# Performance work log

Measured on AMD Instinct MI355X. Metric: run time of the kernel, lower is better.

Reference implementation:

```python
import jax, jax.numpy as jnp
import numpy as np

W = 2  # config.spatial_width in NeuTraj


def _offsets():
    d = np.arange(-W, W + 1)
    dx, dy = np.meshgrid(d, d, indexing='ij')
    return jnp.asarray(np.stack([dx.ravel(), dy.ravel()], axis=1))  # [(2W+1)^2, 2]


def setup_inputs() -> dict:
    key = jax.random.key(0)
    ks = jax.random.split(key, 10)
    B, H, F = 8192, 128, 128
    G = 1100
    N = G + 3 * W  # 1106
    stdv = 1.0 / np.sqrt(H)
    u = lambda k, s: jax.random.uniform(k, s, jnp.float32, -stdv, stdv)
    return {
        'input_feat': jax.random.normal(ks[0], (B, F), jnp.float32),
        'hx': jax.random.normal(ks[1], (B, H), jnp.float32),
        'grid_idx': jax.random.randint(ks[2], (B, 2), 0, G),
        'memory': jax.random.normal(ks[3], (N, N, H), jnp.float32) * 0.1,
        'w_ih': u(ks[4], (4 * H, F)),
        'w_hh': u(ks[5], (4 * H, H)),
        'b_ih': u(ks[6], (4 * H,)),
        'b_hh': u(ks[7], (4 * H,)),
        'w_out': u(ks[8], (H, 2 * H)),  # Attention.linear_out
        'b_out': u(ks[9], (H,)),
    }


def reference(input_feat, hx, grid_idx, memory, w_ih, w_hh, b_ih, b_hh, w_out, b_out):
    g = grid_idx + W  # shift by spatial_width, as in the torch code
    # GRU-style gate GEMMs (4 gates: reset, update, new, spatial)
    gi = input_feat @ w_ih.T + b_ih
    gh = hx @ w_hh.T + b_hh
    i_r, i_i, i_n, i_s = jnp.split(gi, 4, axis=1)
    h_r, h_i, h_n, h_s = jnp.split(gh, 4, axis=1)
    resetgate = jax.nn.sigmoid(i_r + h_r)
    updategate = jax.nn.sigmoid(i_i + h_i)
    spatialgate = jax.nn.sigmoid(i_s + h_s)
    newgate = jnp.tanh(i_n + resetgate * h_n)

    # cy_hh = newgate.data  -> detached attention query
    q = jax.lax.stop_gradient(newgate)

    # gather (2W+1)^2 = 25 neighboring grid cells per sample: cs [B, 25, H]
    nb = g[:, None, :] + _offsets()[None]  # [B, 25, 2]
    cs = memory[nb[..., 0], nb[..., 1]]

    # Luong attention: scores -> softmax -> mix -> concat -> linear -> tanh
    scores = jnp.einsum('bh,blh->bl', q, cs)
    attn = jax.nn.softmax(scores, axis=1)
    mix = jnp.einsum('bl,blh->bh', attn, cs)
    combined = jnp.concatenate([mix, q], axis=1)  # [B, 2H]
    atten_cs = jnp.tanh(combined @ w_out.T + b_out)

    curr_state = newgate + spatialgate * atten_cs
    hyy = curr_state + updategate * (hx - curr_state)

    # incell scatter write-back (all .data in torch -> stop_gradient)
    sg = jax.lax.stop_gradient(spatialgate)
    cd = jax.lax.stop_gradient(hyy)
    gx, gy = g[:, 0], g[:, 1]
    updates = sg * memory[gx, gy] + (1.0 - sg) * cd
    new_memory = memory.at[gx, gy].set(jax.lax.stop_gradient(updates))
    return hyy, new_memory
```

## Files before the change

kernel.cpp:

```cpp
#include <hip/hip_runtime.h>
#include <hip/hip_bf16.h>

typedef float f32x4 __attribute__((ext_vector_type(4)));

#define B_  8192
#define H_  128
#define NW  1106
#define NC  640
#define KK  256

static const size_t N4TOT = (size_t)NW * NW * H_ / 4;

#define SL_A 2000000UL
#define SL_B 6000000UL
#define SL_C 5000000UL
#define SL_D 2000000UL

#define PREP_CB  512
#define PREP_CPB 768
#define GEMM_CPB 1024
#define ATTN_CPB 4096
#define FIN_BLKS 2048

__device__ __forceinline__ float sigmf(float x) { return 1.0f / (1.0f + expf(-x)); }

__device__ __forceinline__ void copy_span(const f32x4* __restrict__ src,
                                          f32x4* __restrict__ dst,
                                          size_t lo, size_t hi,
                                          size_t ctid, size_t cthreads) {
    for (size_t i = lo + ctid; i < hi; i += cthreads) {
        f32x4 v = __builtin_nontemporal_load(src + i);
        __builtin_nontemporal_store(v, dst + i);
    }
}

__global__ __launch_bounds__(256) void prep_kernel(
    const float* __restrict__ xf, const float* __restrict__ hx,
    const float* __restrict__ w_ih, const float* __restrict__ w_hh,
    float* __restrict__ Z, float* __restrict__ Wbig, int* __restrict__ winner,
    const f32x4* __restrict__ src, f32x4* __restrict__ dst, size_t lo, size_t hi) {
    int bid = blockIdx.x, tid = threadIdx.x;
    if (bid >= PREP_CB) {
        size_t ctid = (size_t)(bid - PREP_CB) * 256 + tid;
        copy_span(src, dst, lo, hi, ctid, (size_t)(gridDim.x - PREP_CB) * 256);
        return;
    }
    size_t stride = (size_t)PREP_CB * 256;
    size_t id0 = (size_t)bid * 256 + tid;
    for (size_t i = id0; i < (size_t)B_ * 256; i += stride) {
        size_t b = i >> 8; int c = (int)(i & 255);
        Z[i] = (c < 128) ? xf[b * 128 + c] : hx[b * 128 + (c - 128)];
    }
    for (size_t i = id0; i < (size_t)NC * 256; i += stride) {
        int j = (int)(i >> 8); int k = (int)(i & 255);
        float v;
        if (j < 256) {
            v = (k < 128) ? w_ih[j * 128 + k] : w_hh[j * 128 + (k - 128)];
        } else if (j < 384) {
            int r = 384 + (j - 256);
            v = (k < 128) ? w_ih[r * 128 + k] : w_hh[r * 128 + (k - 128)];
        } else if (j < 512) {
            int r = 256 + (j - 384);
            v = (k < 128) ? w_ih[r * 128 + k] : 0.0f;
        } else {
            int r = 256 + (j - 512);
            v = (k < 128) ? 0.0f : w_hh[r * 128 + (k - 128)];
        }
        Wbig[i] = v;
    }
    for (size_t i = id0; i < (size_t)NW * NW; i += stride) winner[i] = -1;
}

__global__ __launch_bounds__(256) void gemm_abt(
    const float* __restrict__ A, const float* __restrict__ Bw,
    float* __restrict__ Cc, int ldc, int nx, int nxny,
    const int* __restrict__ gidx, int* __restrict__ winner,
    const f32x4* __restrict__ src, f32x4* __restrict__ dst, size_t lo, size_t hi) {
    __shared__ float As[64][36];
    __shared__ float Ws[32][132];
    int bid = blockIdx.x, tid = threadIdx.x;
    if (bid >= nxny) {
        int rel = bid - nxny;
        if (gidx != nullptr && rel < 32) {
            int b = rel * 256 + tid;
            int gx = gidx[2 * b] + 2, gy = gidx[2 * b + 1] + 2;
            atomicMax(&winner[gx * NW + gy], b);
        }
        size_t ctid = (size_t)rel * 256 + tid;
        copy_span(src, dst, lo, hi, ctid, (size_t)(gridDim.x - nxny) * 256);
        return;
    }
    int bx = bid % nx, by = bid / nx;
    int tn = tid & 15, tm = tid >> 4;
    size_t m0 = (size_t)bx * 64;
    int n0 = by * 128;
    float acc[4][8];
#pragma unroll
    for (int i = 0; i < 4; ++i)
#pragma unroll
        for (int j = 0; j < 8; ++j) acc[i][j] = 0.0f;

    for (int k0 = 0; k0 < KK; k0 += 32) {
        __syncthreads();
#pragma unroll
        for (int p = 0; p < 2; ++p) {
            int f = tid + 256 * p; int r = f >> 3, cq = f & 7;
            float4 v = *(const float4*)(A + (m0 + r) * KK + (k0 + 4 * cq));
            *(float4*)(&As[r][4 * cq]) = v;
        }
#pragma unroll
        for (int p = 0; p < 4; ++p) {
            int f = tid + 256 * p; int c = f >> 3, cq = f & 7;
            float4 v = *(const float4*)(Bw + (size_t)(n0 + c) * KK + (k0 + 4 * cq));
            Ws[4 * cq + 0][c] = v.x; Ws[4 * cq + 1][c] = v.y;
            Ws[4 * cq + 2][c] = v.z; Ws[4 * cq + 3][c] = v.w;
        }
        __syncthreads();
#pragma unroll
        for (int kk = 0; kk < 32; ++kk) {
            float4 w0 = *(const float4*)(&Ws[kk][4 * tn]);
            float4 w1 = *(const float4*)(&Ws[kk][64 + 4 * tn]);
#pragma unroll
            for (int i = 0; i < 4; ++i) {
                float a = As[4 * tm + i][kk];
                acc[i][0] += a * w0.x; acc[i][1] += a * w0.y;
                acc[i][2] += a * w0.z; acc[i][3] += a * w0.w;
                acc[i][4] += a * w1.x; acc[i][5] += a * w1.y;
                acc[i][6] += a * w1.z; acc[i][7] += a * w1.w;
            }
        }
    }
#pragma unroll
    for (int i = 0; i < 4; ++i) {
        size_t row = m0 + 4 * tm + i;
        float4 v0 = make_float4(acc[i][0], acc[i][1], acc[i][2], acc[i][3]);
        float4 v1 = make_float4(acc[i][4], acc[i][5], acc[i][6], acc[i][7]);
        *(float4*)(Cc + row * ldc + n0 + 4 * tn) = v0;
        *(float4*)(Cc + row * ldc + n0 + 64 + 4 * tn) = v1;
    }
}

__global__ __launch_bounds__(64) void attn_kernel(
    const float* __restrict__ C, const float* __restrict__ memory,
    const int* __restrict__ gidx, const float* __restrict__ b_ih,
    const float* __restrict__ b_hh, float* __restrict__ mixq,
    float* __restrict__ ug, float* __restrict__ sg,
    const f32x4* __restrict__ src, f32x4* __restrict__ dst, size_t lo, size_t hi) {
    int bid = blockIdx.x;
    int t = threadIdx.x;
    if (bid >= B_) {
        size_t ctid = (size_t)(bid - B_) * 64 + t;
        copy_span(src, dst, lo, hi, ctid, (size_t)(gridDim.x - B_) * 64);
        return;
    }
    int b = bid;
    int t1 = t + 64;
    const float* Crow = C + (size_t)b * NC;
    float r0 = sigmf(Crow[t]        + b_ih[t]        + b_hh[t]);
    float r1 = sigmf(Crow[t1]       + b_ih[t1]       + b_hh[t1]);
    float u0 = sigmf(Crow[128 + t]  + b_ih[128 + t]  + b_hh[128 + t]);
    float u1 = sigmf(Crow[128 + t1] + b_ih[128 + t1] + b_hh[128 + t1]);
    float s0 = sigmf(Crow[256 + t]  + b_ih[384 + t]  + b_hh[384 + t]);
    float s1 = sigmf(Crow[256 + t1] + b_ih[384 + t1] + b_hh[384 + t1]);
    float n0 = tanhf(Crow[384 + t]  + b_ih[256 + t]  + r0 * (Crow[512 + t]  + b_hh[256 + t]));
    float n1 = tanhf(Crow[384 + t1] + b_ih[256 + t1] + r1 * (Crow[512 + t1] + b_hh[256 + t1]));

    int gx = gidx[2 * b] + 2, gy = gidx[2 * b + 1] + 2;
    const float* base = memory + ((size_t)gx * NW + gy) * H_ + t;
    float cs0[25], cs1[25];
#pragma unroll
    for (int l = 0; l < 25; ++l) {
        int dx = l / 5 - 2, dy = l % 5 - 2;
        const float* row = base + ((long)dx * NW + dy) * H_;
        cs0[l] = row[0];
        cs1[l] = row[64];
    }
    float sc[25];
#pragma unroll
    for (int l = 0; l < 25; ++l) {
        float p = n0 * cs0[l] + n1 * cs1[l];
#pragma unroll
        for (int w = 1; w < 64; w <<= 1) p += __shfl_xor(p, w, 64);
        sc[l] = p;
    }
    float mx = sc[0];
#pragma unroll
    for (int l = 1; l < 25; ++l) mx = fmaxf(mx, sc[l]);
    float den = 0.0f, mix0 = 0.0f, mix1 = 0.0f;
#pragma unroll
    for (int l = 0; l < 25; ++l) {
        float e = expf(sc[l] - mx);
        den += e;
        mix0 += e * cs0[l];
        mix1 += e * cs1[l];
    }
    float inv = 1.0f / den;
    mix0 *= inv; mix1 *= inv;

    float* mq = mixq + (size_t)b * 256;
    mq[t] = mix0; mq[t1] = mix1; mq[128 + t] = n0; mq[128 + t1] = n1;
    ug[(size_t)b * H_ + t] = u0; ug[(size_t)b * H_ + t1] = u1;
    sg[(size_t)b * H_ + t] = s0; sg[(size_t)b * H_ + t1] = s1;
}

__global__ void copy_kernel(const f32x4* __restrict__ src, f32x4* __restrict__ dst, size_t n4) {
    size_t stride = (size_t)gridDim.x * blockDim.x;
    for (size_t i = (size_t)blockIdx.x * blockDim.x + threadIdx.x; i < n4; i += stride) {
        f32x4 v = __builtin_nontemporal_load(src + i);
        __builtin_nontemporal_store(v, dst + i);
    }
}

__global__ __launch_bounds__(256) void final_kernel(
    const float* __restrict__ AC, const float* __restrict__ b_out,
    const float* __restrict__ sg, const float* __restrict__ ug,
    const float* __restrict__ mixq, const float* __restrict__ hx,
    const float* __restrict__ memory, const int* __restrict__ gidx,
    const int* __restrict__ winner, float* __restrict__ hyy,
    float* __restrict__ newmem,
    const f32x4* __restrict__ src, f32x4* __restrict__ dst, size_t lo, size_t hi) {
    size_t gt = (size_t)blockIdx.x * blockDim.x + threadIdx.x;
    size_t nthr = (size_t)gridDim.x * blockDim.x;
    for (size_t i = gt; i < (size_t)B_ * H_; i += nthr) {
        int b = (int)(i >> 7), t = (int)(i & 127);
        float atten = tanhf(AC[i] + b_out[t]);
        float s = sg[i], u = ug[i];
        float q = mixq[(size_t)b * 256 + 128 + t];
        float curr = q + s * atten;
        float hy = curr + u * (hx[i] - curr);
        hyy[i] = hy;
        int gx = gidx[2 * b] + 2, gy = gidx[2 * b + 1] + 2;
        size_t cell = (size_t)gx * NW + gy;
        if (winner[cell] == b) {
            float m = memory[cell * H_ + t];
            newmem[cell * H_ + t] = s * m + (1.0f - s) * hy;
        }
    }
    for (size_t i = lo + gt; i < hi; i += nthr) {
        if (winner[i >> 5] < 0) {
            f32x4 v = __builtin_nontemporal_load(src + i);
            __builtin_nontemporal_store(v, dst + i);
        }
    }
}

extern "C" void kernel_launch(void* const* d_in, const int* in_sizes, int n_in,
                              void* d_out, int out_size, void* d_ws, size_t ws_size,
                              hipStream_t stream) {
    const float* xf     = (const float*)d_in[0];
    const float* hx     = (const float*)d_in[1];
    const int*   gidx   = (const int*)d_in[2];
    const float* memory = (const float*)d_in[3];
    const float* w_ih   = (const float*)d_in[4];
    const float* w_hh   = (const float*)d_in[5];
    const float* b_ih   = (const float*)d_in[6];
    const float* b_hh   = (const float*)d_in[7];
    const float* w_out  = (const float*)d_in[8];
    const float* b_out  = (const float*)d_in[9];

    float* out    = (float*)d_out;
    float* hyy    = out;
    float* newmem = out + (size_t)B_ * H_;
    const f32x4* src4 = (const f32x4*)memory;
    f32x4*       dst4 = (f32x4*)newmem;

    float* wsf    = (float*)d_ws;
    float* mixq   = wsf;
    float* ug     = mixq + (size_t)B_ * 256;
    float* sg     = ug + (size_t)B_ * H_;
    float* AC     = sg + (size_t)B_ * H_;
    int*   winner = (int*)(AC + (size_t)B_ * H_);
    char*  pers_end = (char*)(winner + (size_t)NW * NW);
    size_t pers_bytes = (size_t)(pers_end - (char*)d_ws);

    size_t ZF = (size_t)B_ * 256, CF = (size_t)B_ * NC, WBF = (size_t)NC * 256;
    size_t trans_bytes = (ZF + CF + WBF) * sizeof(float);
    bool distributed = (ws_size >= pers_bytes + trans_bytes);
    float* trans = distributed ? (float*)pers_end : newmem;
    float* Z    = trans;
    float* Cbuf = Z + ZF;
    float* Wbig = Cbuf + CF;

    if (distributed) {
        size_t a1 = SL_A, b1 = a1 + SL_B, c1 = b1 + SL_C, d1 = c1 + SL_D;
        prep_kernel<<<PREP_CB + PREP_CPB, 256, 0, stream>>>(
            xf, hx, w_ih, w_hh, Z, Wbig, winner, src4, dst4, 0, a1);
        gemm_abt<<<640 + GEMM_CPB, 256, 0, stream>>>(
            Z, Wbig, Cbuf, NC, 128, 640, gidx, winner, src4, dst4, a1, b1);
        attn_kernel<<<B_ + ATTN_CPB, 64, 0, stream>>>(
            Cbuf, memory, gidx, b_ih, b_hh, mixq, ug, sg, src4, dst4, b1, c1);
        gemm_abt<<<128 + GEMM_CPB, 256, 0, stream>>>(
            mixq, w_out, AC, H_, 128, 128, nullptr, winner, src4, dst4, c1, d1);
        final_kernel<<<FIN_BLKS, 256, 0, stream>>>(
            AC, b_out, sg, ug, mixq, hx, memory, gidx, winner, hyy, newmem,
            src4, dst4, d1, N4TOT);
    } else {
        prep_kernel<<<PREP_CB, 256, 0, stream>>>(
            xf, hx, w_ih, w_hh, Z, Wbig, winner, src4, dst4, 0, 0);
        gemm_abt<<<640 + 32, 256, 0, stream>>>(
            Z, Wbig, Cbuf, NC, 128, 640, gidx, winner, src4, dst4, 0, 0);
        attn_kernel<<<B_, 64, 0, stream>>>(
            Cbuf, memory, gidx, b_ih, b_hh, mixq, ug, sg, src4, dst4, 0, 0);
        gemm_abt<<<128, 256, 0, stream>>>(
            mixq, w_out, AC, H_, 128, 128, nullptr, winner, src4, dst4, 0, 0);
        copy_kernel<<<2048, 256, 0, stream>>>(src4, dst4, N4TOT);
        final_kernel<<<FIN_BLKS, 256, 0, stream>>>(
            AC, b_out, sg, ug, mixq, hx, memory, gidx, winner, hyy, newmem,
            src4, dst4, 0, 0);
    }
}
```

Baseline: 281.9 us.

## Collapse five-stage pipeline into three kernels with fused GEMM epilogues

After: 333.5 us. 18.3% more time.

```diff
diff --git a/kernel.cpp b/kernel.cpp
--- a/kernel.cpp
+++ b/kernel.cpp
@@ -11,16 +11,13 @@
 
 static const size_t N4TOT = (size_t)NW * NW * H_ / 4;
 
-#define SL_A 2000000UL
-#define SL_B 6000000UL
-#define SL_C 5000000UL
-#define SL_D 2000000UL
-
-#define PREP_CB  512
-#define PREP_CPB 768
-#define GEMM_CPB 1024
-#define ATTN_CPB 4096
-#define FIN_BLKS 2048
+#define SL1 6000000UL
+#define SL2 4000000UL
+
+#define K1_CPB 1024
+#define K2_CB  2048
+#define K2_CPB 1024
+#define K3_CPB 2048
 
 __device__ __forceinline__ float sigmf(float x) { return 1.0f / (1.0f + expf(-x)); }
 
@@ -34,84 +31,57 @@
     }
 }
 
-__global__ __launch_bounds__(256) void prep_kernel(
+__global__ __launch_bounds__(256) void k1_gates(
     const float* __restrict__ xf, const float* __restrict__ hx,
     const float* __restrict__ w_ih, const float* __restrict__ w_hh,
-    float* __restrict__ Z, float* __restrict__ Wbig, int* __restrict__ winner,
-    const f32x4* __restrict__ src, f32x4* __restrict__ dst, size_t lo, size_t hi) {
-    int bid = blockIdx.x, tid = threadIdx.x;
-    if (bid >= PREP_CB) {
-        size_t ctid = (size_t)(bid - PREP_CB) * 256 + tid;
-        copy_span(src, dst, lo, hi, ctid, (size_t)(gridDim.x - PREP_CB) * 256);
-        return;
-    }
-    size_t stride = (size_t)PREP_CB * 256;
-    size_t id0 = (size_t)bid * 256 + tid;
-    for (size_t i = id0; i < (size_t)B_ * 256; i += stride) {
-        size_t b = i >> 8; int c = (int)(i & 255);
-        Z[i] = (c < 128) ? xf[b * 128 + c] : hx[b * 128 + (c - 128)];
-    }
-    for (size_t i = id0; i < (size_t)NC * 256; i += stride) {
-        int j = (int)(i >> 8); int k = (int)(i & 255);
-        float v;
-        if (j < 256) {
-            v = (k < 128) ? w_ih[j * 128 + k] : w_hh[j * 128 + (k - 128)];
-        } else if (j < 384) {
-            int r = 384 + (j - 256);
-            v = (k < 128) ? w_ih[r * 128 + k] : w_hh[r * 128 + (k - 128)];
-        } else if (j < 512) {
-            int r = 256 + (j - 384);
-            v = (k < 128) ? w_ih[r * 128 + k] : 0.0f;
-        } else {
-            int r = 256 + (j - 512);
-            v = (k < 128) ? 0.0f : w_hh[r * 128 + (k - 128)];
-        }
-        Wbig[i] = v;
-    }
-    for (size_t i = id0; i < (size_t)NW * NW; i += stride) winner[i] = -1;
-}
-
-__global__ __launch_bounds__(256) void gemm_abt(
-    const float* __restrict__ A, const float* __restrict__ Bw,
-    float* __restrict__ Cc, int ldc, int nx, int nxny,
-    const int* __restrict__ gidx, int* __restrict__ winner,
+    float* __restrict__ Cbuf, const int* __restrict__ gidx, int* __restrict__ winner,
     const f32x4* __restrict__ src, f32x4* __restrict__ dst, size_t lo, size_t hi) {
     __shared__ float As[64][36];
     __shared__ float Ws[32][132];
     int bid = blockIdx.x, tid = threadIdx.x;
-    if (bid >= nxny) {
-        int rel = bid - nxny;
-        if (gidx != nullptr && rel < 32) {
+    if (bid >= 640) {
+        int rel = bid - 640;
+        if (rel < 32) {
             int b = rel * 256 + tid;
             int gx = gidx[2 * b] + 2, gy = gidx[2 * b + 1] + 2;
             atomicMax(&winner[gx * NW + gy], b);
         }
         size_t ctid = (size_t)rel * 256 + tid;
-        copy_span(src, dst, lo, hi, ctid, (size_t)(gridDim.x - nxny) * 256);
+        copy_span(src, dst, lo, hi, ctid, (size_t)(gridDim.x - 640) * 256);
         return;
     }
-    int bx = bid % nx, by = bid / nx;
+    int bx = bid & 127;
+    int strip = bid >> 7;
+    size_t m0 = (size_t)bx * 64;
+    int n0 = strip * 128;
+    int wbase = (strip == 0) ? 0 : (strip == 1) ? 128 : (strip == 2) ? 384 : 256;
+    int kstart = (strip == 4) ? 128 : 0;
+    int kend   = (strip == 3) ? 128 : 256;
+
     int tn = tid & 15, tm = tid >> 4;
-    size_t m0 = (size_t)bx * 64;
-    int n0 = by * 128;
     float acc[4][8];
 #pragma unroll
     for (int i = 0; i < 4; ++i)
 #pragma unroll
         for (int j = 0; j < 8; ++j) acc[i][j] = 0.0f;
 
-    for (int k0 = 0; k0 < KK; k0 += 32) {
+    for (int k0 = kstart; k0 < kend; k0 += 32) {
+        const float* asrc = (k0 < 128) ? xf : hx;
+        const float* wsrc = (strip == 3) ? w_ih
+                          : (strip == 4) ? w_hh
+                          : (k0 < 128 ? w_ih : w_hh);
+        int koff = k0 & 127;
         __syncthreads();
 #pragma unroll
         for (int p = 0; p < 2; ++p) {
             int f = tid + 256 * p; int r = f >> 3, cq = f & 7;
-            float4 v = *(const float4*)(A + (m0 + r) * KK + (k0 + 4 * cq));
+            float4 v = *(const float4*)(asrc + (m0 + r) * 128 + koff + 4 * cq);
             *(float4*)(&As[r][4 * cq]) = v;
         }
 #pragma unroll
         for (int p = 0; p < 4; ++p) {
             int f = tid + 256 * p; int c = f >> 3, cq = f & 7;
-            float4 v = *(const float4*)(Bw + (size_t)(n0 + c) * KK + (k0 + 4 * cq));
+            float4 v = *(const float4*)(wsrc + (size_t)(wbase + c) * 128 + koff + 4 * cq);
             Ws[4 * cq + 0][c] = v.x; Ws[4 * cq + 1][c] = v.y;
             Ws[4 * cq + 2][c] = v.z; Ws[4 * cq + 3][c] = v.w;
         }
@@ -135,25 +105,25 @@
         size_t row = m0 + 4 * tm + i;
         float4 v0 = make_float4(acc[i][0], acc[i][1], acc[i][2], acc[i][3]);
         float4 v1 = make_float4(acc[i][4], acc[i][5], acc[i][6], acc[i][7]);
-        *(float4*)(Cc + row * ldc + n0 + 4 * tn) = v0;
-        *(float4*)(Cc + row * ldc + n0 + 64 + 4 * tn) = v1;
-    }
-}
-
-__global__ __launch_bounds__(64) void attn_kernel(
+        *(float4*)(Cbuf + row * NC + n0 + 4 * tn) = v0;
+        *(float4*)(Cbuf + row * NC + n0 + 64 + 4 * tn) = v1;
+    }
+}
+
+__global__ __launch_bounds__(256) void k2_attn(
     const float* __restrict__ C, const float* __restrict__ memory,
     const int* __restrict__ gidx, const float* __restrict__ b_ih,
     const float* __restrict__ b_hh, float* __restrict__ mixq,
     float* __restrict__ ug, float* __restrict__ sg,
     const f32x4* __restrict__ src, f32x4* __restrict__ dst, size_t lo, size_t hi) {
-    int bid = blockIdx.x;
-    int t = threadIdx.x;
-    if (bid >= B_) {
-        size_t ctid = (size_t)(bid - B_) * 64 + t;
-        copy_span(src, dst, lo, hi, ctid, (size_t)(gridDim.x - B_) * 64);
+    int bid = blockIdx.x, tid = threadIdx.x;
+    if (bid >= K2_CB) {
+        size_t ctid = (size_t)(bid - K2_CB) * 256 + tid;
+        copy_span(src, dst, lo, hi, ctid, (size_t)(gridDim.x - K2_CB) * 256);
         return;
     }
-    int b = bid;
+    int b = bid * 4 + (tid >> 6);
+    int t = tid & 63;
     int t1 = t + 64;
     const float* Crow = C + (size_t)b * NC;
     float r0 = sigmf(Crow[t]        + b_ih[t]        + b_hh[t]);
@@ -203,44 +173,99 @@
     sg[(size_t)b * H_ + t] = s0; sg[(size_t)b * H_ + t1] = s1;
 }
 
+__global__ __launch_bounds__(256) void k3_final(
+    const float* __restrict__ mixq, const float* __restrict__ w_out,
+    const float* __restrict__ b_out, const float* __restrict__ sg,
+    const float* __restrict__ ug, const float* __restrict__ hx,
+    const float* __restrict__ memory, const int* __restrict__ gidx,
+    const int* __restrict__ winner, float* __restrict__ hyy,
+    float* __restrict__ newmem,
+    const f32x4* __restrict__ src, f32x4* __restrict__ dst, size_t lo, size_t hi) {
+    __shared__ float As[64][36];
+    __shared__ float Ws[32][132];
+    int bid = blockIdx.x, tid = threadIdx.x;
+    if (bid >= 128) {
+        size_t ctid = (size_t)(bid - 128) * 256 + tid;
+        size_t nthr = (size_t)(gridDim.x - 128) * 256;
+        for (size_t i = lo + ctid; i < hi; i += nthr) {
+            if (winner[i >> 5] < 0) {
+                f32x4 v = __builtin_nontemporal_load(src + i);
+                __builtin_nontemporal_store(v, dst + i);
+            }
+        }
+        return;
+    }
+    size_t m0 = (size_t)bid * 64;
+    int tn = tid & 15, tm = tid >> 4;
+    float acc[4][8];
+#pragma unroll
+    for (int i = 0; i < 4; ++i)
+#pragma unroll
+        for (int j = 0; j < 8; ++j) acc[i][j] = 0.0f;
+
+    for (int k0 = 0; k0 < KK; k0 += 32) {
+        __syncthreads();
+#pragma unroll
+        for (int p = 0; p < 2; ++p) {
+            int f = tid + 256 * p; int r = f >> 3, cq = f & 7;
+            float4 v = *(const float4*)(mixq + (m0 + r) * KK + k0 + 4 * cq);
+            *(float4*)(&As[r][4 * cq]) = v;
+        }
+#pragma unroll
+        for (int p = 0; p < 4; ++p) {
+            int f = tid + 256 * p; int c = f >> 3, cq = f & 7;
+            float4 v = *(const float4*)(w_out + (size_t)c * KK + k0 + 4 * cq);
+            Ws[4 * cq + 0][c] = v.x; Ws[4 * cq + 1][c] = v.y;
+            Ws[4 * cq + 2][c] = v.z; Ws[4 * cq + 3][c] = v.w;
+        }
+        __syncthreads();
+#pragma unroll
+        for (int kk = 0; kk < 32; ++kk) {
+            float4 w0 = *(const float4*)(&Ws[kk][4 * tn]);
+            float4 w1 = *(const float4*)(&Ws[kk][64 + 4 * tn]);
+#pragma unroll
+            for (int i = 0; i < 4; ++i) {
+                float a = As[4 * tm + i][kk];
+                acc[i][0] += a * w0.x; acc[i][1] += a * w0.y;
+                acc[i][2] += a * w0.z; acc[i][3] += a * w0.w;
+                acc[i][4] += a * w1.x; acc[i][5] += a * w1.y;
+                acc[i][6] += a * w1.z; acc[i][7] += a * w1.w;
+            }
+        }
+    }
+#pragma unroll
+    for (int i = 0; i < 4; ++i) {
+        size_t row = m0 + 4 * tm + i;
+        int gx = gidx[2 * row] + 2, gy = gidx[2 * row + 1] + 2;
+        size_t cell = (size_t)gx * NW + gy;
+        bool win = (winner[cell] == (int)row);
+#pragma unroll
+        for (int half = 0; half < 2; ++half) {
+#pragma unroll
+            for (int j = 0; j < 4; ++j) {
+                int col = half * 64 + 4 * tn + j;
+                float a = acc[i][half * 4 + j];
+                float atten = tanhf(a + b_out[col]);
+                float s = sg[row * H_ + col];
+                float u = ug[row * H_ + col];
+                float q = mixq[row * 256 + 128 + col];
+                float curr = q + s * atten;
+                float hy = curr + u * (hx[row * H_ + col] - curr);
+                hyy[row * H_ + col] = hy;
+                if (win) {
+                    float m = memory[cell * H_ + col];
+                    newmem[cell * H_ + col] = s * m + (1.0f - s) * hy;
+                }
+            }
+        }
+    }
+}
+
 __global__ void copy_kernel(const f32x4* __restrict__ src, f32x4* __restrict__ dst, size_t n4) {
     size_t stride = (size_t)gridDim.x * blockDim.x;
     for (size_t i = (size_t)blockIdx.x * blockDim.x + threadIdx.x; i < n4; i += stride) {
         f32x4 v = __builtin_nontemporal_load(src + i);
         __builtin_nontemporal_store(v, dst + i);
-    }
-}
-
-__global__ __launch_bounds__(256) void final_kernel(
-    const float* __restrict__ AC, const float* __restrict__ b_out,
-    const float* __restrict__ sg, const float* __restrict__ ug,
-    const float* __restrict__ mixq, const float* __restrict__ hx,
-    const float* __restrict__ memory, const int* __restrict__ gidx,
-    const int* __restrict__ winner, float* __restrict__ hyy,
-    float* __restrict__ newmem,
-    const f32x4* __restrict__ src, f32x4* __restrict__ dst, size_t lo, size_t hi) {
-    size_t gt = (size_t)blockIdx.x * blockDim.x + threadIdx.x;
-    size_t nthr = (size_t)gridDim.x * blockDim.x;
-    for (size_t i = gt; i < (size_t)B_ * H_; i += nthr) {
-        int b = (int)(i >> 7), t = (int)(i & 127);
-        float atten = tanhf(AC[i] + b_out[t]);
-        float s = sg[i], u = ug[i];
-        float q = mixq[(size_t)b * 256 + 128 + t];
-        float curr = q + s * atten;
-        float hy = curr + u * (hx[i] - curr);
-        hyy[i] = hy;
-        int gx = gidx[2 * b] + 2, gy = gidx[2 * b + 1] + 2;
-        size_t cell = (size_t)gx * NW + gy;
-        if (winner[cell] == b) {
-            float m = memory[cell * H_ + t];
-            newmem[cell * H_ + t] = s * m + (1.0f - s) * hy;
-        }
-    }
-    for (size_t i = lo + gt; i < hi; i += nthr) {
-        if (winner[i >> 5] < 0) {
-            f32x4 v = __builtin_nontemporal_load(src + i);
-            __builtin_nontemporal_store(v, dst + i);
-        }
     }
 }
 
@@ -268,44 +293,33 @@
     float* mixq   = wsf;
     float* ug     = mixq + (size_t)B_ * 256;
     float* sg     = ug + (size_t)B_ * H_;
-    float* AC     = sg + (size_t)B_ * H_;
-    int*   winner = (int*)(AC + (size_t)B_ * H_);
+    int*   winner = (int*)(sg + (size_t)B_ * H_);
     char*  pers_end = (char*)(winner + (size_t)NW * NW);
     size_t pers_bytes = (size_t)(pers_end - (char*)d_ws);
 
-    size_t ZF = (size_t)B_ * 256, CF = (size_t)B_ * NC, WBF = (size_t)NC * 256;
-    size_t trans_bytes = (ZF + CF + WBF) * sizeof(float);
-    bool distributed = (ws_size >= pers_bytes + trans_bytes);
-    float* trans = distributed ? (float*)pers_end : newmem;
-    float* Z    = trans;
-    float* Cbuf = Z + ZF;
-    float* Wbig = Cbuf + CF;
+    size_t CF = (size_t)B_ * NC;
+    bool distributed = (ws_size >= pers_bytes + CF * sizeof(float));
+    float* Cbuf = distributed ? (float*)pers_end : newmem;
+
+    hipMemsetAsync(winner, 0xFF, (size_t)NW * NW * sizeof(int), stream);
 
     if (distributed) {
-        size_t a1 = SL_A, b1 = a1 + SL_B, c1 = b1 + SL_C, d1 = c1 + SL_D;
-        prep_kernel<<<PREP_CB + PREP_CPB, 256, 0, stream>>>(
-            xf, hx, w_ih, w_hh, Z, Wbig, winner, src4, dst4, 0, a1);
-        gemm_abt<<<640 + GEMM_CPB, 256, 0, stream>>>(
-            Z, Wbig, Cbuf, NC, 128, 640, gidx, winner, src4, dst4, a1, b1);
-        attn_kernel<<<B_ + ATTN_CPB, 64, 0, stream>>>(
-            Cbuf, memory, gidx, b_ih, b_hh, mixq, ug, sg, src4, dst4, b1, c1);
-        gemm_abt<<<128 + GEMM_CPB, 256, 0, stream>>>(
-            mixq, w_out, AC, H_, 128, 128, nullptr, winner, src4, dst4, c1, d1);
-        final_kernel<<<FIN_BLKS, 256, 0, stream>>>(
-            AC, b_out, sg, ug, mixq, hx, memory, gidx, winner, hyy, newmem,
-            src4, dst4, d1, N4TOT);
+        size_t a1 = SL1, b1 = a1 + SL2;
+        k1_gates<<<640 + K1_CPB, 256, 0, stream>>>(
+            xf, hx, w_ih, w_hh, Cbuf, gidx, winner, src4, dst4, 0, a1);
+        k2_attn<<<K2_CB + K2_CPB, 256, 0, stream>>>(
+            Cbuf, memory, gidx, b_ih, b_hh, mixq, ug, sg, src4, dst4, a1, b1);
+        k3_final<<<128 + K3_CPB, 256, 0, stream>>>(
+            mixq, w_out, b_out, sg, ug, hx, memory, gidx, winner, hyy, newmem,
+            src4, dst4, b1, N4TOT);
     } else {
-        prep_kernel<<<PREP_CB, 256, 0, stream>>>(
-            xf, hx, w_ih, w_hh, Z, Wbig, winner, src4, dst4, 0, 0);
-        gemm_abt<<<640 + 32, 256, 0, stream>>>(
-            Z, Wbig, Cbuf, NC, 128, 640, gidx, winner, src4, dst4, 0, 0);
-        attn_kernel<<<B_, 64, 0, stream>>>(
+        k1_gates<<<640 + 32, 256, 0, stream>>>(
+            xf, hx, w_ih, w_hh, Cbuf, gidx, winner, src4, dst4, 0, 0);
+        k2_attn<<<K2_CB, 256, 0, stream>>>(
             Cbuf, memory, gidx, b_ih, b_hh, mixq, ug, sg, src4, dst4, 0, 0);
-        gemm_abt<<<128, 256, 0, stream>>>(
-            mixq, w_out, AC, H_, 128, 128, nullptr, winner, src4, dst4, 0, 0);
         copy_kernel<<<2048, 256, 0, stream>>>(src4, dst4, N4TOT);
-        final_kernel<<<FIN_BLKS, 256, 0, stream>>>(
-            AC, b_out, sg, ug, mixq, hx, memory, gidx, winner, hyy, newmem,
+        k3_final<<<128 + 32, 256, 0, stream>>>(
+            mixq, w_out, b_out, sg, ug, hx, memory, gidx, winner, hyy, newmem,
             src4, dst4, 0, 0);
     }
 }
```

## Read GEMM operands directly from xf/hx, drop Z staging, transpose A in LDS

Applied to the files above, without the earlier changes.

New measurement: 286.0 us. Within noise of the previous version (+1.4%).

```diff
diff --git a/kernel.cpp b/kernel.cpp
--- a/kernel.cpp
+++ b/kernel.cpp
@@ -11,13 +11,13 @@
 
 static const size_t N4TOT = (size_t)NW * NW * H_ / 4;
 
-#define SL_A 2000000UL
-#define SL_B 6000000UL
+#define SL_A 1500000UL
+#define SL_B 7000000UL
 #define SL_C 5000000UL
-#define SL_D 2000000UL
-
-#define PREP_CB  512
-#define PREP_CPB 768
+#define SL_D 2500000UL
+
+#define PREP_CB  256
+#define PREP_CPB 1024
 #define GEMM_CPB 1024
 #define ATTN_CPB 4096
 #define FIN_BLKS 2048
@@ -35,9 +35,8 @@
 }
 
 __global__ __launch_bounds__(256) void prep_kernel(
-    const float* __restrict__ xf, const float* __restrict__ hx,
     const float* __restrict__ w_ih, const float* __restrict__ w_hh,
-    float* __restrict__ Z, float* __restrict__ Wbig, int* __restrict__ winner,
+    float* __restrict__ Wbig, int* __restrict__ winner,
     const f32x4* __restrict__ src, f32x4* __restrict__ dst, size_t lo, size_t hi) {
     int bid = blockIdx.x, tid = threadIdx.x;
     if (bid >= PREP_CB) {
@@ -47,10 +46,6 @@
     }
     size_t stride = (size_t)PREP_CB * 256;
     size_t id0 = (size_t)bid * 256 + tid;
-    for (size_t i = id0; i < (size_t)B_ * 256; i += stride) {
-        size_t b = i >> 8; int c = (int)(i & 255);
-        Z[i] = (c < 128) ? xf[b * 128 + c] : hx[b * 128 + (c - 128)];
-    }
     for (size_t i = id0; i < (size_t)NC * 256; i += stride) {
         int j = (int)(i >> 8); int k = (int)(i & 255);
         float v;
@@ -72,11 +67,13 @@
 }
 
 __global__ __launch_bounds__(256) void gemm_abt(
-    const float* __restrict__ A, const float* __restrict__ Bw,
-    float* __restrict__ Cc, int ldc, int nx, int nxny,
+    const float* __restrict__ A0, int lda0,
+    const float* __restrict__ A1, int lda1,
+    const float* __restrict__ Bw, float* __restrict__ Cc, int ldc,
+    int nx, int nxny,
     const int* __restrict__ gidx, int* __restrict__ winner,
     const f32x4* __restrict__ src, f32x4* __restrict__ dst, size_t lo, size_t hi) {
-    __shared__ float As[64][36];
+    __shared__ float As[32][68];
     __shared__ float Ws[32][132];
     int bid = blockIdx.x, tid = threadIdx.x;
     if (bid >= nxny) {
@@ -101,12 +98,16 @@
         for (int j = 0; j < 8; ++j) acc[i][j] = 0.0f;
 
     for (int k0 = 0; k0 < KK; k0 += 32) {
+        const float* a0 = (k0 < 128) ? A0 : A1;
+        int lda = (k0 < 128) ? lda0 : lda1;
+        int koff = k0 & 127;
         __syncthreads();
 #pragma unroll
         for (int p = 0; p < 2; ++p) {
             int f = tid + 256 * p; int r = f >> 3, cq = f & 7;
-            float4 v = *(const float4*)(A + (m0 + r) * KK + (k0 + 4 * cq));
-            *(float4*)(&As[r][4 * cq]) = v;
+            float4 v = *(const float4*)(a0 + (size_t)(m0 + r) * lda + koff + 4 * cq);
+            As[4 * cq + 0][r] = v.x; As[4 * cq + 1][r] = v.y;
+            As[4 * cq + 2][r] = v.z; As[4 * cq + 3][r] = v.w;
         }
 #pragma unroll
         for (int p = 0; p < 4; ++p) {
@@ -118,15 +119,16 @@
         __syncthreads();
 #pragma unroll
         for (int kk = 0; kk < 32; ++kk) {
+            float4 a4 = *(const float4*)(&As[kk][4 * tm]);
             float4 w0 = *(const float4*)(&Ws[kk][4 * tn]);
             float4 w1 = *(const float4*)(&Ws[kk][64 + 4 * tn]);
+            float a_[4] = {a4.x, a4.y, a4.z, a4.w};
 #pragma unroll
             for (int i = 0; i < 4; ++i) {
-                float a = As[4 * tm + i][kk];
-                acc[i][0] += a * w0.x; acc[i][1] += a * w0.y;
-                acc[i][2] += a * w0.z; acc[i][3] += a * w0.w;
-                acc[i][4] += a * w1.x; acc[i][5] += a * w1.y;
-                acc[i][6] += a * w1.z; acc[i][7] += a * w1.w;
+                acc[i][0] += a_[i] * w0.x; acc[i][1] += a_[i] * w0.y;
+                acc[i][2] += a_[i] * w0.z; acc[i][3] += a_[i] * w0.w;
+                acc[i][4] += a_[i] * w1.x; acc[i][5] += a_[i] * w1.y;
+                acc[i][6] += a_[i] * w1.z; acc[i][7] += a_[i] * w1.w;
             }
         }
     }
@@ -273,36 +275,39 @@
     char*  pers_end = (char*)(winner + (size_t)NW * NW);
     size_t pers_bytes = (size_t)(pers_end - (char*)d_ws);
 
-    size_t ZF = (size_t)B_ * 256, CF = (size_t)B_ * NC, WBF = (size_t)NC * 256;
-    size_t trans_bytes = (ZF + CF + WBF) * sizeof(float);
+    size_t CF = (size_t)B_ * NC, WBF = (size_t)NC * 256;
+    size_t trans_bytes = (CF + WBF) * sizeof(float);
     bool distributed = (ws_size >= pers_bytes + trans_bytes);
     float* trans = distributed ? (float*)pers_end : newmem;
-    float* Z    = trans;
-    float* Cbuf = Z + ZF;
+    float* Cbuf = trans;
     float* Wbig = Cbuf + CF;
 
     if (distributed) {
         size_t a1 = SL_A, b1 = a1 + SL_B, c1 = b1 + SL_C, d1 = c1 + SL_D;
         prep_kernel<<<PREP_CB + PREP_CPB, 256, 0, stream>>>(
-            xf, hx, w_ih, w_hh, Z, Wbig, winner, src4, dst4, 0, a1);
+            w_ih, w_hh, Wbig, winner, src4, dst4, 0, a1);
         gemm_abt<<<640 + GEMM_CPB, 256, 0, stream>>>(
-            Z, Wbig, Cbuf, NC, 128, 640, gidx, winner, src4, dst4, a1, b1);
+            xf, 128, hx, 128, Wbig, Cbuf, NC, 128, 640, gidx, winner,
+            src4, dst4, a1, b1);
         attn_kernel<<<B_ + ATTN_CPB, 64, 0, stream>>>(
             Cbuf, memory, gidx, b_ih, b_hh, mixq, ug, sg, src4, dst4, b1, c1);
         gemm_abt<<<128 + GEMM_CPB, 256, 0, stream>>>(
-            mixq, w_out, AC, H_, 128, 128, nullptr, winner, src4, dst4, c1, d1);
+            mixq, 256, mixq + 128, 256, w_out, AC, H_, 128, 128, nullptr, winner,
+            src4, dst4, c1, d1);
         final_kernel<<<FIN_BLKS, 256, 0, stream>>>(
             AC, b_out, sg, ug, mixq, hx, memory, gidx, winner, hyy, newmem,
             src4, dst4, d1, N4TOT);
     } else {
         prep_kernel<<<PREP_CB, 256, 0, stream>>>(
-            xf, hx, w_ih, w_hh, Z, Wbig, winner, src4, dst4, 0, 0);
+            w_ih, w_hh, Wbig, winner, src4, dst4, 0, 0);
         gemm_abt<<<640 + 32, 256, 0, stream>>>(
-            Z, Wbig, Cbuf, NC, 128, 640, gidx, winner, src4, dst4, 0, 0);
+            xf, 128, hx, 128, Wbig, Cbuf, NC, 128, 640, gidx, winner,
+            src4, dst4, 0, 0);
         attn_kernel<<<B_, 64, 0, stream>>>(
             Cbuf, memory, gidx, b_ih, b_hh, mixq, ug, sg, src4, dst4, 0, 0);
         gemm_abt<<<128, 256, 0, stream>>>(
-            mixq, w_out, AC, H_, 128, 128, nullptr, winner, src4, dst4, 0, 0);
+            mixq, 256, mixq + 128, 256, w_out, AC, H_, 128, 128, nullptr, winner,
+            src4, dst4, 0, 0);
         copy_kernel<<<2048, 256, 0, stream>>>(src4, dst4, N4TOT);
         final_kernel<<<FIN_BLKS, 256, 0, stream>>>(
             AC, b_out, sg, ug, mixq, hx, memory, gidx, winner, hyy, newmem,
```
